# Performance work log

Measured on AMD Instinct MI355X. Metric: run time of the kernel, lower is better.

The kernel has to match this reference:

```python
import jax, jax.numpy as jnp
import numpy as np

B, N, D_DELTA, D_EVT, F, H, L = 4, 2048, 1, 384, 128, 4, 2
NEG_BIG = -9e15

def _gelu(x):
    return jax.nn.gelu(x, approximate=False)

def setup_inputs() -> dict:
    key = jax.random.key(0)
    ks = jax.random.split(key, 32)
    def glorot(k, shape, gain=1.0):
        fan_in, fan_out = shape[-2], shape[-1]
        lim = gain * np.sqrt(6.0 / (fan_in + fan_out))
        return jax.random.uniform(k, shape, jnp.float32, -lim, lim)
    inp = {}
    inp['deltas'] = jax.random.normal(ks[0], (B, N, D_DELTA), jnp.float32)
    inp['event_embeddings'] = jax.random.normal(ks[1], (B, N, D_EVT), jnp.float32)
    u = jax.random.uniform(ks[2], (B, N, N), jnp.float32)
    inp['trade_adjacency'] = jnp.where(u > 0.9, u, 0.0)
    din = D_DELTA + D_EVT
    # message network: din->F, F->F, F->F
    inp['mw1'] = glorot(ks[3], (din, F)); inp['mb1'] = jnp.zeros((F,))
    inp['mw2'] = glorot(ks[4], (F, F));   inp['mb2'] = jnp.zeros((F,))
    inp['mw3'] = glorot(ks[5], (F, F));   inp['mb3'] = jnp.zeros((F,))
    # gate network: din->F//2 -> F
    inp['gw1'] = glorot(ks[6], (din, F // 2)); inp['gb1'] = jnp.zeros((F // 2,))
    inp['gw2'] = glorot(ks[7], (F // 2, F));   inp['gb2'] = jnp.zeros((F,))
    # GAT params per layer/head: W (L,H,F,F), attention vec a split into src/dst halves
    inp['Wg'] = glorot(ks[8], (L, H, F, F), gain=1.414)
    a = glorot(ks[9], (L, H, 2 * F, 1), gain=1.414)
    inp['a_src'] = a[:, :, :F, 0]  # (L,H,F)
    inp['a_dst'] = a[:, :, F:, 0]  # (L,H,F)
    # per-layer head-concat output projection: (L, H*F, F)
    inp['pw'] = glorot(ks[10], (L, H * F, F)); inp['pb'] = jnp.zeros((L, F))
    # output projection: F -> F//2 -> delta_dim
    inp['ow1'] = glorot(ks[11], (F, F // 2)); inp['ob1'] = jnp.zeros((F // 2,))
    inp['ow2'] = glorot(ks[12], (F // 2, D_DELTA)); inp['ob2'] = jnp.zeros((D_DELTA,))
    inp['alpha_param'] = jnp.full((N, D_DELTA), 0.5, jnp.float32)
    inp['beta'] = jnp.asarray(1.0, jnp.float32)
    return inp

def reference(deltas, event_embeddings, trade_adjacency,
              mw1, mb1, mw2, mb2, mw3, mb3, gw1, gb1, gw2, gb2,
              Wg, a_src, a_dst, pw, pb, ow1, ob1, ow2, ob2,
              alpha_param, beta):
    # message function phi(delta, E): gated MLP (eval mode, dropout off)
    combined = jnp.concatenate([deltas, event_embeddings], axis=-1)  # (B,N,din)
    m = _gelu(combined @ mw1 + mb1)
    m = _gelu(m @ mw2 + mb2)
    m = m @ mw3 + mb3
    g = _gelu(combined @ gw1 + gb1)
    g = jax.nn.sigmoid(g @ gw2 + gb2)
    h = m * g  # (B,N,F)
    adj_pos = trade_adjacency[:, None] > 0  # (B,1,N,N)
    for l in range(L):
        Wh = jnp.einsum('bnf,hfo->bhno', h, Wg[l])             # (B,H,N,F)
        s = jnp.einsum('bhno,ho->bhn', Wh, a_src[l])           # score contrib of node i
        t = jnp.einsum('bhno,ho->bhn', Wh, a_dst[l])           # score contrib of node j
        e = jax.nn.leaky_relu(s[:, :, :, None] + t[:, :, None, :], 0.2)  # (B,H,N,N)
        e = jnp.where(adj_pos, e, NEG_BIG)
        attn = jax.nn.softmax(e, axis=-1)
        hp = jax.nn.elu(jnp.einsum('bhij,bhjo->bhio', attn, Wh))  # (B,H,N,F)
        h = hp.transpose(0, 2, 1, 3).reshape(B, N, H * F) @ pw[l] + pb[l]  # (B,N,F)
    prop = _gelu(h @ ow1 + ob1) @ ow2 + ob2                     # (B,N,delta_dim)
    deltas_next = jax.nn.sigmoid(alpha_param)[None] * deltas + beta * prop
    return deltas_next
```

## Files before the change

kernel.cpp:

```cpp
#include <hip/hip_runtime.h>
#include <hip/hip_bf16.h>
#include <math.h>

#define B_ 4
#define N_ 2048
#define F_ 128
#define H_ 4
#define NEG_BIG_F -9.0e15f

typedef float v2 __attribute__((ext_vector_type(2)));
typedef float v4 __attribute__((ext_vector_type(4)));
typedef float f32x16 __attribute__((ext_vector_type(16)));
typedef short s16x8 __attribute__((ext_vector_type(8)));
typedef short s16x4 __attribute__((ext_vector_type(4)));
typedef unsigned u32x4 __attribute__((ext_vector_type(4)));
typedef unsigned u32x2 __attribute__((ext_vector_type(2)));

__device__ __forceinline__ float gelu_f(float x){
  return 0.5f*x*(1.0f+erff(x*0.70710678118654752f));
}
__device__ __forceinline__ float sigmoid_f(float x){
  return 1.0f/(1.0f+__expf(-x));
}
__device__ __forceinline__ short bfbits(float v){
  __hip_bfloat16 h = __float2bfloat16(v);
  short r; __builtin_memcpy(&r, &h, 2); return r;
}
__device__ __forceinline__ float bfback(short s){
  return __uint_as_float(((unsigned)(unsigned short)s) << 16);
}
__device__ __forceinline__ unsigned packhi(float a, float b){
  return __builtin_amdgcn_perm(__float_as_uint(b), __float_as_uint(a), 0x07060302u);
}
__device__ __forceinline__ unsigned cvtpk_bf16(float a, float b){
  unsigned r;
  asm("v_cvt_pk_bf16_f32 %0, %1, %2" : "=v"(r) : "v"(a), "v"(b));
  return r;
}

__global__ void __launch_bounds__(256) mask_kernel(
    const float* __restrict__ adj, unsigned* __restrict__ maskT)
{
  int v = blockIdx.x;
  int b = v >> 6; int n0 = (v & 63) * 32;
  int t = threadIdx.x;
  int r = t >> 3, jg = t & 7;
  __shared__ unsigned mw[32][65];
  const float* arow = adj + (size_t)(b*N_ + n0 + r)*N_;
  for (int wq=0; wq<8; wq++){
    int wdi = jg + 8*wq;
    unsigned bits = 0;
    #pragma unroll
    for (int m=0;m<8;m++){
      v4 a = *(const v4*)(arow + wdi*32 + m*4);
      bits |= (a.x>0.f?1u:0u)<<(m*4);
      bits |= (a.y>0.f?1u:0u)<<(m*4+1);
      bits |= (a.z>0.f?1u:0u)<<(m*4+2);
      bits |= (a.w>0.f?1u:0u)<<(m*4+3);
    }
    mw[r][wdi] = bits;
  }
  __syncthreads();
  #pragma unroll
  for (int q=0;q<8;q++){
    int idx = t + q*256;
    int wdi = idx >> 5, rr = idx & 31;
    maskT[((size_t)b*64 + wdi)*N_ + n0 + rr] = mw[rr][wdi];
  }
}

__global__ void __launch_bounds__(192) w1m_kernel(
    const float* __restrict__ mw1, const float* __restrict__ gw1,
    float* __restrict__ w1m)
{
  int k = blockIdx.x;
  int c = threadIdx.x;
  w1m[(size_t)k*192 + c] = (c < 128) ? mw1[(size_t)k*128 + c]
                                     : gw1[(size_t)k*64 + (c-128)];
}

__global__ void __launch_bounds__(256) mlp1_kernel(
    const float* __restrict__ deltas, const float* __restrict__ evt,
    const float* __restrict__ w1m,
    const float* __restrict__ mb1, const float* __restrict__ gb1,
    float* __restrict__ s1ws)
{
  int row0 = blockIdx.x * 8;
  int t = threadIdx.x;
  int w = t >> 6, l = t & 63;
  int tcol = l & 31, rhalf = l >> 5;
  int c0 = tcol * 6;
  __shared__ float xs[8][392];
  __shared__ float pacc[4][8][192];

  for (int idx = t; idx < 8*385; idx += 256){
    int i = idx / 385;
    int k = idx - i*385;
    xs[i][k] = (k==0) ? deltas[row0+i] : evt[(size_t)(row0+i)*384 + (k-1)];
  }
  __syncthreads();

  int kstart = (w*385) >> 2, kend = ((w+1)*385) >> 2;
  float acc[4][6];
  #pragma unroll
  for (int r=0;r<4;r++)
    #pragma unroll
    for (int e=0;e<6;e++) acc[r][e] = 0.f;

  #pragma unroll 4
  for (int k=kstart; k<kend; k++){
    const float* wp = w1m + (size_t)k*192 + c0;
    v2 wa = *(const v2*)wp;
    v2 wb = *(const v2*)(wp+2);
    v2 wc = *(const v2*)(wp+4);
    #pragma unroll
    for (int r=0;r<4;r++){
      float x = xs[rhalf*4+r][k];
      acc[r][0] += x*wa.x; acc[r][1] += x*wa.y;
      acc[r][2] += x*wb.x; acc[r][3] += x*wb.y;
      acc[r][4] += x*wc.x; acc[r][5] += x*wc.y;
    }
  }
  #pragma unroll
  for (int r=0;r<4;r++){
    float* pp = &pacc[w][rhalf*4+r][c0];
    #pragma unroll
    for (int e=0;e<6;e++) pp[e] = acc[r][e];
  }
  __syncthreads();

  int row = t >> 5, cc0 = (t & 31) * 6;
  #pragma unroll
  for (int e=0;e<6;e++){
    int c = cc0 + e;
    float s = pacc[0][row][c] + pacc[1][row][c] + pacc[2][row][c] + pacc[3][row][c];
    s += (c < 128) ? mb1[c] : gb1[c-128];
    s1ws[(size_t)(row0+row)*192 + c] = gelu_f(s);
  }
}

__global__ void __launch_bounds__(256) mlp2_kernel(
    const float* __restrict__ s1ws,
    const float* __restrict__ mw2, const float* __restrict__ mb2,
    const float* __restrict__ mw3, const float* __restrict__ mb3,
    const float* __restrict__ gw2, const float* __restrict__ gb2,
    float* __restrict__ h_out)
{
  int row0 = blockIdx.x * 8;
  int t = threadIdx.x;
  int w = t >> 6, l = t & 63;
  int tcol = l & 31, rhalf = l >> 5;
  int c0 = tcol * 4;

  __shared__ float sm[1600 + 2048 + 2048 + 1024];
  float (*xs)[200] = (float(*)[200])sm;
  float* mpart = sm + 1600;
  float* gpart = sm + 1600 + 2048;
  float* xs2   = sm + 1600 + 4096;
  float* p3    = sm + 1600;

  for (int idx = t; idx < 8*48; idx += 256){
    int i = idx / 48, c4 = idx - i*48;
    *(v4*)&xs[i][c4*4] = *(const v4*)(s1ws + (size_t)(row0+i)*192 + c4*4);
  }
  __syncthreads();

  {
    v4 acc[4];
    #pragma unroll
    for (int r=0;r<4;r++) acc[r] = (v4)0.f;
    if (w < 2){
      int ks2 = w*64;
      #pragma unroll 4
      for (int k=ks2; k<ks2+64; k++){
        v4 wv = *(const v4*)(mw2 + (size_t)k*128 + c0);
        #pragma unroll
        for (int r=0;r<4;r++) acc[r] += xs[rhalf*4+r][k]*wv;
      }
      #pragma unroll
      for (int r=0;r<4;r++)
        *(v4*)&mpart[((size_t)w*8 + rhalf*4+r)*128 + c0] = acc[r];
    } else {
      int ks2 = (w-2)*32;
      #pragma unroll 4
      for (int k=ks2; k<ks2+32; k++){
        v4 wv = *(const v4*)(gw2 + (size_t)k*128 + c0);
        #pragma unroll
        for (int r=0;r<4;r++) acc[r] += xs[rhalf*4+r][128+k]*wv;
      }
      #pragma unroll
      for (int r=0;r<4;r++)
        *(v4*)&gpart[((size_t)(w-2)*8 + rhalf*4+r)*128 + c0] = acc[r];
    }
  }
  __syncthreads();

  int row = t >> 5, cb = (t & 31) * 4;
  v4 gp;
  {
    v4 m2 = *(const v4*)&mpart[(size_t)row*128 + cb];
    m2 += *(const v4*)&mpart[(size_t)(8+row)*128 + cb];
    m2 += *(const v4*)(mb2 + cb);
    gp = *(const v4*)&gpart[(size_t)row*128 + cb];
    gp += *(const v4*)&gpart[(size_t)(8+row)*128 + cb];
    gp += *(const v4*)(gb2 + cb);
    v4 o;
    o.x = gelu_f(m2.x); o.y = gelu_f(m2.y); o.z = gelu_f(m2.z); o.w = gelu_f(m2.w);
    __syncthreads();
    *(v4*)&xs2[(size_t)row*128 + cb] = o;
  }
  __syncthreads();

  {
    v4 acc3[4];
    #pragma unroll
    for (int r=0;r<4;r++) acc3[r] = (v4)0.f;
    int kc = w*32;
    #pragma unroll 4
    for (int k=kc; k<kc+32; k++){
      v4 wv = *(const v4*)(mw3 + (size_t)k*128 + c0);
      #pragma unroll
      for (int r=0;r<4;r++) acc3[r] += xs2[(size_t)(rhalf*4+r)*128 + k]*wv;
    }
    #pragma unroll
    for (int r=0;r<4;r++)
      *(v4*)&p3[((size_t)w*8 + rhalf*4+r)*128 + c0] = acc3[r];
  }
  __syncthreads();

  {
    v4 s = *(const v4*)&p3[(size_t)row*128 + cb];
    s += *(const v4*)&p3[(size_t)(8+row)*128 + cb];
    s += *(const v4*)&p3[(size_t)(16+row)*128 + cb];
    s += *(const v4*)&p3[(size_t)(24+row)*128 + cb];
    s += *(const v4*)(mb3 + cb);
    v4 o;
    o.x = s.x * sigmoid_f(gp.x);
    o.y = s.y * sigmoid_f(gp.y);
    o.z = s.z * sigmoid_f(gp.z);
    o.w = s.w * sigmoid_f(gp.w);
    *(v4*)(h_out + (size_t)(row0+row)*F_ + cb) = o;
  }
}

__global__ void __launch_bounds__(256) wh_kernel(
    const float* __restrict__ h,
    const float* __restrict__ Wg_l,
    const float* __restrict__ asrc_l,
    const float* __restrict__ adst_l,
    short* __restrict__ WhT_hi,
    float* __restrict__ sArr,
    float* __restrict__ tArr)
{
  int v = blockIdx.x;
  int itile = v & 31;
  int bh = v >> 5;
  int b = bh >> 2, hh = bh & 3;
  int n0 = itile * 64;
  int t = threadIdx.x;
  int i0  = (t & 7) * 8;
  int fo0 = (t >> 3) * 4;

  __shared__ float hT[128][72];
  __shared__ float sP[4][64], tP[4][64];
  for (int idx = t; idx < 64*128; idx += 256){
    int i = idx >> 7, k = idx & 127;
    hT[k][i] = h[(size_t)(b*N_ + n0 + i)*F_ + k];
  }
  __syncthreads();

  const float* W = Wg_l + (size_t)hh*F_*F_;
  v4 accA[4], accB[4];
  #pragma unroll
  for (int c=0;c<4;c++){ accA[c]=(v4)0.f; accB[c]=(v4)0.f; }
  #pragma unroll 4
  for (int k=0;k<F_;k++){
    v4 w = *(const v4*)(W + (size_t)k*F_ + fo0);
    v4 ha = *(const v4*)&hT[k][i0];
    v4 hb = *(const v4*)&hT[k][i0+4];
    accA[0]+=w.x*ha; accA[1]+=w.y*ha; accA[2]+=w.z*ha; accA[3]+=w.w*ha;
    accB[0]+=w.x*hb; accB[1]+=w.y*hb; accB[2]+=w.z*hb; accB[3]+=w.w*hb;
  }
  #pragma unroll
  for (int c=0;c<4;c++){
    s16x8 hi8;
    #pragma unroll
    for (int e=0;e<8;e++){
      float x = (e<4) ? accA[c][e] : accB[c][e-4];
      hi8[e] = bfbits(x);
    }
    size_t off = ((size_t)bh*F_ + fo0 + c)*N_ + n0 + i0;
    *(s16x8*)(WhT_hi + off) = hi8;
  }
  v4 as4 = *(const v4*)(asrc_l + hh*F_ + fo0);
  v4 ad4 = *(const v4*)(adst_l + hh*F_ + fo0);
  v4 sva = accA[0]*as4.x + accA[1]*as4.y + accA[2]*as4.z + accA[3]*as4.w;
  v4 svb = accB[0]*as4.x + accB[1]*as4.y + accB[2]*as4.z + accB[3]*as4.w;
  v4 tva = accA[0]*ad4.x + accA[1]*ad4.y + accA[2]*ad4.z + accA[3]*ad4.w;
  v4 tvb = accB[0]*ad4.x + accB[1]*ad4.y + accB[2]*ad4.z + accB[3]*ad4.w;
  #pragma unroll
  for (int m=8;m<=32;m<<=1){
    sva.x+=__shfl_xor(sva.x,m); sva.y+=__shfl_xor(sva.y,m); sva.z+=__shfl_xor(sva.z,m); sva.w+=__shfl_xor(sva.w,m);
    svb.x+=__shfl_xor(svb.x,m); svb.y+=__shfl_xor(svb.y,m); svb.z+=__shfl_xor(svb.z,m); svb.w+=__shfl_xor(svb.w,m);
    tva.x+=__shfl_xor(tva.x,m); tva.y+=__shfl_xor(tva.y,m); tva.z+=__shfl_xor(tva.z,m); tva.w+=__shfl_xor(tva.w,m);
    tvb.x+=__shfl_xor(tvb.x,m); tvb.y+=__shfl_xor(tvb.y,m); tvb.z+=__shfl_xor(tvb.z,m); tvb.w+=__shfl_xor(tvb.w,m);
  }
  int wv = t >> 6;
  if ((t & 56) == 0){
    *(v4*)&sP[wv][i0] = sva; *(v4*)&sP[wv][i0+4] = svb;
    *(v4*)&tP[wv][i0] = tva; *(v4*)&tP[wv][i0+4] = tvb;
  }
  __syncthreads();
  if (t < 64){
    sArr[(size_t)bh*N_ + n0 + t] = sP[0][t]+sP[1][t]+sP[2][t]+sP[3][t];
    tArr[(size_t)bh*N_ + n0 + t] = tP[0][t]+tP[1][t]+tP[2][t]+tP[3][t];
  }
}

#define WHS 44
#define PBS 18
__global__ void __launch_bounds__(512) attn_kernel(
    const unsigned* __restrict__ maskT,
    const short* __restrict__ WhT_hi,
    const float* __restrict__ sArr,
    const float* __restrict__ tArr,
    float* __restrict__ hpWS)
{
  int v = blockIdx.x;
  int seq = v >> 3, x8 = v & 7;
  int bh = (seq >> 5)*8 + x8;
  int itile = seq & 31;
  int b = bh >> 2;
  int n0 = itile * 64;
  int t = threadIdx.x;
  int w = t >> 6, l = t & 63;
  int lg = l >> 5, ln = l & 31;
  int ihalf = w & 1;
  int ks    = (w >> 1) & 1;
  int fhalf = w >> 2;

  __shared__ float tvecL[N_];
  __shared__ short whHiL[2][128*WHS];
  __shared__ unsigned pbufHi[2][2][32][PBS];
  __shared__ unsigned pbufLo[2][2][32][PBS];
  __shared__ float mxPart[8][64];
  __shared__ float mxL[64], amArgL[64], invL[64];
  __shared__ float lsP[2][4][32];

  const float* tp = tArr + (size_t)bh*N_;
  #pragma unroll
  for (int q=0;q<4;q++) tvecL[t + q*512] = tp[t + q*512];

  s16x8 rh;
  int srow = t >> 2, sseg = t & 3;
  const short* gHi = WhT_hi + (size_t)bh*F_*N_;
  auto STAGE = [&](int jj0){
    size_t o = (size_t)srow*N_ + jj0 + sseg*8;
    rh = *(const s16x8*)(gHi + o);
  };
  auto WRITE = [&](int buf){
    int wo = srow*WHS + sseg*8;
    *(s16x4*)&whHiL[buf][wo]   = __builtin_shufflevector(rh,rh,0,1,2,3);
    *(s16x4*)&whHiL[buf][wo+4] = __builtin_shufflevector(rh,rh,4,5,6,7);
  };

  STAGE(0);
  int il = t & 63, qq = t >> 6;
  float s_il = sArr[(size_t)bh*N_ + n0 + il];
  __syncthreads();

  float mx = NEG_BIG_F;
  const unsigned* mb1p = maskT + (size_t)b*64*N_ + n0;
  for (int wq=0; wq<8; wq++){
    int wdi = qq + wq*8;
    unsigned wd = mb1p[(size_t)wdi*N_ + il];
    while (wd){
      int k2 = __builtin_ctz(wd); wd &= wd - 1;
      float e = s_il + tvecL[wdi*32 + k2];
      e = fmaxf(e, 0.2f*e);
      mx = fmaxf(mx, e);
    }
  }
  mxPart[qq][il] = mx;
  WRITE(0);
  __syncthreads();
  if (t < 64){
    float m = mxPart[0][t];
    #pragma unroll
    for (int q=1;q<8;q++) m = fmaxf(m, mxPart[q][t]);
    bool am = (m <= -8.0e15f);
    mxL[t] = am ? 0.f : m;
    amArgL[t] = am ? 0.f : -1.0e30f;
  }
  __syncthreads();

  int irow = n0 + ihalf*32 + ln;
  float s_lane  = sArr[(size_t)bh*N_ + irow];
  float mx_lane = mxL[ihalf*32 + ln];
  float amArg_lane = amArgL[ihalf*32 + ln];
  const unsigned* mrow = maskT + (size_t)b*64*N_ + irow;

  f32x16 acc0, acc1;
  #pragma unroll
  for (int e2=0;e2<16;e2++){ acc0[e2]=0.f; acc1[e2]=0.f; }
  float lsum = 0.f;

  int jsub = ks*16 + fhalf*8 + lg*4;
  int qidx = jsub >> 1;
  int sh0 = ks*16 + lg*8;

  unsigned mword = mrow[0];
  for (int c=0;c<64;c++){
    int j0 = c*32;
    int cb = c & 1;
    unsigned mword_nx = (c<63) ? mrow[(size_t)(c+1)*N_] : 0u;
    if (c<63) STAGE(j0 + 32);

    {
      v4 tv4 = *(const v4*)&tvecL[j0 + jsub];
      unsigned mm = mword >> jsub;
      float pe0, pe1, pe2, pe3;
      {
        float ev = s_lane + tv4.x; ev = fmaxf(ev, 0.2f*ev);
        pe0 = __expf((mm & 1u) ? (ev - mx_lane) : amArg_lane);
        ev = s_lane + tv4.y; ev = fmaxf(ev, 0.2f*ev);
        pe1 = __expf(((mm>>1) & 1u) ? (ev - mx_lane) : amArg_lane);
        ev = s_lane + tv4.z; ev = fmaxf(ev, 0.2f*ev);
        pe2 = __expf(((mm>>2) & 1u) ? (ev - mx_lane) : amArg_lane);
        ev = s_lane + tv4.w; ev = fmaxf(ev, 0.2f*ev);
        pe3 = __expf(((mm>>3) & 1u) ? (ev - mx_lane) : amArg_lane);
      }
      lsum += (pe0+pe1)+(pe2+pe3);
      u32x2 hiP, loP;
      hiP[0] = packhi(pe0, pe1);
      hiP[1] = packhi(pe2, pe3);
      float l0 = pe0 - __uint_as_float(__float_as_uint(pe0)&0xffff0000u);
      float l1 = pe1 - __uint_as_float(__float_as_uint(pe1)&0xffff0000u);
      float l2 = pe2 - __uint_as_float(__float_as_uint(pe2)&0xffff0000u);
      float l3 = pe3 - __uint_as_float(__float_as_uint(pe3)&0xffff0000u);
      loP[0] = cvtpk_bf16(l0, l1);
      loP[1] = cvtpk_bf16(l2, l3);
      *(u32x2*)&pbufHi[cb][ihalf][ln][qidx] = hiP;
      *(u32x2*)&pbufLo[cb][ihalf][ln][qidx] = loP;
    }
    __syncthreads();

    {
      int aq0 = ks*8 + lg*4;
      u32x2 ha2 = *(const u32x2*)&pbufHi[cb][ihalf][ln][aq0];
      u32x2 hb2 = *(const u32x2*)&pbufHi[cb][ihalf][ln][aq0+2];
      u32x2 la2 = *(const u32x2*)&pbufLo[cb][ihalf][ln][aq0];
      u32x2 lb2 = *(const u32x2*)&pbufLo[cb][ihalf][ln][aq0+2];
      u32x4 h4; h4[0]=ha2[0]; h4[1]=ha2[1]; h4[2]=hb2[0]; h4[3]=hb2[1];
      u32x4 l4; l4[0]=la2[0]; l4[1]=la2[1]; l4[2]=lb2[0]; l4[3]=lb2[1];
      s16x8 ahi = __builtin_bit_cast(s16x8, h4);
      s16x8 alo = __builtin_bit_cast(s16x8, l4);
      __builtin_amdgcn_s_setprio(1);
      #pragma unroll
      for (int aq=0; aq<2; aq++){
        int fr = fhalf*64 + aq*32 + ln;
        const short* bp = &whHiL[cb][fr*WHS + sh0];
        s16x4 b0 = *(const s16x4*)bp;
        s16x4 b1 = *(const s16x4*)(bp+4);
        s16x8 bhi = __builtin_shufflevector(b0,b1,0,1,2,3,4,5,6,7);
        if (aq == 0){
          acc0 = __builtin_amdgcn_mfma_f32_32x32x16_bf16(ahi, bhi, acc0, 0,0,0);
          acc0 = __builtin_amdgcn_mfma_f32_32x32x16_bf16(alo, bhi, acc0, 0,0,0);
        } else {
          acc1 = __builtin_amdgcn_mfma_f32_32x32x16_bf16(ahi, bhi, acc1, 0,0,0);
          acc1 = __builtin_amdgcn_mfma_f32_32x32x16_bf16(alo, bhi, acc1, 0,0,0);
        }
      }
      __builtin_amdgcn_s_setprio(0);
    }
    if (c<63) WRITE(cb ^ 1);
    mword = mword_nx;
  }

  lsum += __shfl_xor(lsum, 32);
  if (l < 32) lsP[ihalf][ks*2+fhalf][l] = lsum;

  float* redbuf = tvecL;
  __syncthreads();
  #pragma unroll
  for (int ihr=0; ihr<2; ihr++){
    if (ks==1 && ihalf==ihr){
      #pragma unroll
      for (int e=0;e<16;e++) redbuf[(fhalf*64 + l)*16 + e] = acc0[e];
    }
    __syncthreads();
    if (ks==0 && ihalf==ihr){
      #pragma unroll
      for (int e=0;e<16;e++) acc0[e] += redbuf[(fhalf*64 + l)*16 + e];
    }
    __syncthreads();
    if (ks==1 && ihalf==ihr){
      #pragma unroll
      for (int e=0;e<16;e++) redbuf[(fhalf*64 + l)*16 + e] = acc1[e];
    }
    __syncthreads();
    if (ks==0 && ihalf==ihr){
      #pragma unroll
      for (int e=0;e<16;e++) acc1[e] += redbuf[(fhalf*64 + l)*16 + e];
    }
    __syncthreads();
  }

  if (t < 64){
    int ih2 = t >> 5, lr = t & 31;
    float s4 = lsP[ih2][0][lr] + lsP[ih2][1][lr] + lsP[ih2][2][lr] + lsP[ih2][3][lr];
    invL[t] = 1.0f / s4;
  }
  __syncthreads();

  if (ks == 0){
    float* hpb = hpWS + ((size_t)bh*N_ + n0 + ihalf*32)*F_ + fhalf*64 + ln;
    #pragma unroll
    for (int q4=0;q4<4;q4++){
      #pragma unroll
      for (int rr=0;rr<4;rr++){
        int r = q4*4+rr;
        int irl = rr + 8*q4 + 4*lg;
        float inv = invL[ihalf*32 + irl];
        float v0 = acc0[r]*inv;
        v0 = v0 > 0.f ? v0 : expm1f(v0);
        hpb[(size_t)irl*F_] = v0;
        float v1 = acc1[r]*inv;
        v1 = v1 > 0.f ? v1 : expm1f(v1);
        hpb[(size_t)irl*F_ + 32] = v1;
      }
    }
  }
}

__global__ void __launch_bounds__(256) proj_kernel(
    const float* __restrict__ hpWS,
    const float* __restrict__ pw_l,
    const float* __restrict__ pb_l,
    float* __restrict__ h_out)
{
  int v = blockIdx.x;
  int b = v >> 8;
  int n0 = (v & 255) * 8;
  int t = threadIdx.x;
  int w = t >> 6, l = t & 63;
  int tcol = l & 31, rhalf = l >> 5;
  int c0 = tcol * 4;

  __shared__ float xsp[4][8][128];
  __shared__ float pacc[4][8][128];
  for (int idx = t; idx < 1024; idx += 256){
    int kh = idx >> 8, r = (idx >> 5) & 7, f4 = idx & 31;
    *(v4*)&xsp[kh][r][f4*4] =
      *(const v4*)(hpWS + ((size_t)(b*H_+kh)*N_ + n0 + r)*F_ + f4*4);
  }
  __syncthreads();

  v4 acc[4];
  #pragma unroll
  for (int r=0;r<4;r++) acc[r] = (v4)0.f;
  const float* pwk = pw_l + (size_t)w*128*F_;
  #pragma unroll 4
  for (int k=0;k<128;k++){
    v4 wv = *(const v4*)(pwk + (size_t)k*F_ + c0);
    #pragma unroll
    for (int r=0;r<4;r++) acc[r] += xsp[w][rhalf*4+r][k]*wv;
  }
  #pragma unroll
  for (int r=0;r<4;r++)
    *(v4*)&pacc[w][rhalf*4+r][c0] = acc[r];
  __syncthreads();

  int row = t >> 5, cb = (t & 31)*4;
  v4 s = *(const v4*)&pacc[0][row][cb];
  s += *(const v4*)&pacc[1][row][cb];
  s += *(const v4*)&pacc[2][row][cb];
  s += *(const v4*)&pacc[3][row][cb];
  s += *(const v4*)(pb_l + cb);
  *(v4*)(h_out + (size_t)(b*N_ + n0 + row)*F_ + cb) = s;
}

__global__ void __launch_bounds__(256) out_kernel(
    const float* __restrict__ h,
    const float* __restrict__ deltas,
    const float* __restrict__ alpha,
    const float* __restrict__ beta,
    const float* __restrict__ ow1, const float* __restrict__ ob1,
    const float* __restrict__ ow2, const float* __restrict__ ob2,
    float* __restrict__ out)
{
  int row0 = blockIdx.x * 32;
  int t = threadIdx.x;
  int il = t >> 3, fg = t & 7;
  int f0 = fg * 8;
  __shared__ float hL[32][132];
  for (int idx = t; idx < 32*128; idx += 256){
    int i = idx >> 7, k = idx & 127;
    hL[i][k] = h[(size_t)(row0+i)*F_ + k];
  }
  __syncthreads();
  float acc[8];
  #pragma unroll
  for (int q=0;q<8;q++) acc[q] = ob1[f0+q];
  for (int k=0;k<F_;k++){
    float c = hL[il][k];
    const float* w = ow1 + (size_t)k*64 + f0;
    v4 wa = *(const v4*)w; v4 wb = *(const v4*)(w+4);
    acc[0]+=c*wa.x; acc[1]+=c*wa.y; acc[2]+=c*wa.z; acc[3]+=c*wa.w;
    acc[4]+=c*wb.x; acc[5]+=c*wb.y; acc[6]+=c*wb.z; acc[7]+=c*wb.w;
  }
  float pp = 0.f;
  #pragma unroll
  for (int q=0;q<8;q++) pp += gelu_f(acc[q]) * ow2[f0+q];
  pp += __shfl_xor(pp, 1);
  pp += __shfl_xor(pp, 2);
  pp += __shfl_xor(pp, 4);
  if (fg == 0){
    int row = row0 + il;
    int n = row & (N_-1);
    float prop = pp + ob2[0];
    out[row] = sigmoid_f(alpha[n]) * deltas[row] + beta[0]*prop;
  }
}

extern "C" void kernel_launch(void* const* d_in, const int* in_sizes, int n_in,
                              void* d_out, int out_size, void* d_ws, size_t ws_size,
                              hipStream_t stream) {
  const float* deltas = (const float*)d_in[0];
  const float* evt    = (const float*)d_in[1];
  const float* adj    = (const float*)d_in[2];
  const float* mw1 = (const float*)d_in[3];
  const float* mb1 = (const float*)d_in[4];
  const float* mw2 = (const float*)d_in[5];
  const float* mb2 = (const float*)d_in[6];
  const float* mw3 = (const float*)d_in[7];
  const float* mb3 = (const float*)d_in[8];
  const float* gw1 = (const float*)d_in[9];
  const float* gb1 = (const float*)d_in[10];
  const float* gw2 = (const float*)d_in[11];
  const float* gb2 = (const float*)d_in[12];
  const float* Wg  = (const float*)d_in[13];
  const float* a_src = (const float*)d_in[14];
  const float* a_dst = (const float*)d_in[15];
  const float* pw = (const float*)d_in[16];
  const float* pb = (const float*)d_in[17];
  const float* ow1 = (const float*)d_in[18];
  const float* ob1 = (const float*)d_in[19];
  const float* ow2 = (const float*)d_in[20];
  const float* ob2 = (const float*)d_in[21];
  const float* alpha = (const float*)d_in[22];
  const float* beta  = (const float*)d_in[23];
  float* out = (float*)d_out;

  float* ws = (float*)d_ws;
  float* hA = ws;
  float* hB = hA + (size_t)B_*N_*F_;
  short* WhT_hi = (short*)(hB + (size_t)B_*N_*F_);
  short* WhT_lo = WhT_hi + (size_t)B_*H_*F_*N_;
  float* hp = (float*)(WhT_lo + (size_t)B_*H_*F_*N_);
  float* sA = hp + (size_t)B_*H_*N_*F_;
  float* tA = sA + (size_t)B_*H_*N_;
  unsigned* maskT = (unsigned*)(tA + (size_t)B_*H_*N_);
  float* w1m = (float*)(maskT + (size_t)B_*64*N_);
  float* s1ws = hp;

  int BN = B_*N_;
  w1m_kernel<<<385, 192, 0, stream>>>(mw1, gw1, w1m);
  mask_kernel<<<B_*64, 256, 0, stream>>>(adj, maskT);
  mlp1_kernel<<<BN/8, 256, 0, stream>>>(deltas, evt, w1m, mb1, gb1, s1ws);
  mlp2_kernel<<<BN/8, 256, 0, stream>>>(s1ws, mw2, mb2, mw3, mb3, gw2, gb2, hA);
  const float* hin = hA; float* hout = hB;
  for (int l=0;l<2;l++){
    wh_kernel<<<16*32, 256, 0, stream>>>(hin,
        Wg + (size_t)l*H_*F_*F_, a_src + (size_t)l*H_*F_, a_dst + (size_t)l*H_*F_,
        WhT_hi, sA, tA);
    attn_kernel<<<512, 512, 0, stream>>>(maskT, WhT_hi, sA, tA, hp);
    proj_kernel<<<1024, 256, 0, stream>>>(hp,
        pw + (size_t)l*H_*F_*F_, pb + (size_t)l*F_, hout);
    float* tmp = (float*)hin; hin = hout; hout = tmp;
  }
  out_kernel<<<BN/32, 256, 0, stream>>>(hin, deltas, alpha, beta, ow1, ob1, ow2, ob2, out);
}
```

Baseline: 295.9 us.

## Fold log2e into attention scores and halve wh_kernel tile for more blocks

In the attention kernel, the t vector is stored twice in shared memory, prescaled by log2e and by 0.2*log2e. Leaky-relu then becomes a max of two affine terms, and the softmax exponent uses raw v_exp_f32 with the row max folded into per-lane constants, which removes multiplies and the expf scaling from the inner loop. Separately, wh_kernel now uses 32-row tiles with 4x4 per-thread outputs and twice as many blocks, aiming for more parallelism on the GPU. The extra t2L array doubles that shared-memory footprint and may reduce occupancy, and each wh block reloads W for fewer rows.

```diff
diff --git a/kernel.cpp b/kernel.cpp
--- a/kernel.cpp
+++ b/kernel.cpp
@@ -7,6 +7,7 @@
 #define F_ 128
 #define H_ 4
 #define NEG_BIG_F -9.0e15f
+#define L2E 1.44269504088896f
 
 typedef float v2 __attribute__((ext_vector_type(2)));
 typedef float v4 __attribute__((ext_vector_type(4)));
@@ -26,15 +27,17 @@
   __hip_bfloat16 h = __float2bfloat16(v);
   short r; __builtin_memcpy(&r, &h, 2); return r;
 }
-__device__ __forceinline__ float bfback(short s){
-  return __uint_as_float(((unsigned)(unsigned short)s) << 16);
-}
 __device__ __forceinline__ unsigned packhi(float a, float b){
   return __builtin_amdgcn_perm(__float_as_uint(b), __float_as_uint(a), 0x07060302u);
 }
 __device__ __forceinline__ unsigned cvtpk_bf16(float a, float b){
   unsigned r;
   asm("v_cvt_pk_bf16_f32 %0, %1, %2" : "=v"(r) : "v"(a), "v"(b));
+  return r;
+}
+__device__ __forceinline__ float exp2_f(float x){
+  float r;
+  asm("v_exp_f32 %0, %1" : "=v"(r) : "v"(x));
   return r;
 }
 
@@ -253,65 +256,63 @@
     float* __restrict__ tArr)
 {
   int v = blockIdx.x;
-  int itile = v & 31;
-  int bh = v >> 5;
+  int itile = v & 63;
+  int bh = v >> 6;
   int b = bh >> 2, hh = bh & 3;
-  int n0 = itile * 64;
+  int n0 = itile * 32;
   int t = threadIdx.x;
-  int i0  = (t & 7) * 8;
-  int fo0 = (t >> 3) * 4;
-
-  __shared__ float hT[128][72];
-  __shared__ float sP[4][64], tP[4][64];
-  for (int idx = t; idx < 64*128; idx += 256){
+  int w = t >> 6;
+  int ig = t & 7;
+  int fg = t >> 3;
+  int i0 = ig*4, f0 = fg*4;
+
+  __shared__ float hT[128][36];
+  __shared__ float sP[4][32], tP[4][32];
+  for (int idx = t; idx < 32*128; idx += 256){
     int i = idx >> 7, k = idx & 127;
     hT[k][i] = h[(size_t)(b*N_ + n0 + i)*F_ + k];
   }
   __syncthreads();
 
   const float* W = Wg_l + (size_t)hh*F_*F_;
-  v4 accA[4], accB[4];
-  #pragma unroll
-  for (int c=0;c<4;c++){ accA[c]=(v4)0.f; accB[c]=(v4)0.f; }
+  v4 acc[4];
+  #pragma unroll
+  for (int r=0;r<4;r++) acc[r] = (v4)0.f;
   #pragma unroll 4
   for (int k=0;k<F_;k++){
-    v4 w = *(const v4*)(W + (size_t)k*F_ + fo0);
-    v4 ha = *(const v4*)&hT[k][i0];
-    v4 hb = *(const v4*)&hT[k][i0+4];
-    accA[0]+=w.x*ha; accA[1]+=w.y*ha; accA[2]+=w.z*ha; accA[3]+=w.w*ha;
-    accB[0]+=w.x*hb; accB[1]+=w.y*hb; accB[2]+=w.z*hb; accB[3]+=w.w*hb;
+    v4 wv = *(const v4*)(W + (size_t)k*F_ + f0);
+    v4 hv = *(const v4*)&hT[k][i0];
+    acc[0] += hv.x*wv; acc[1] += hv.y*wv; acc[2] += hv.z*wv; acc[3] += hv.w*wv;
   }
   #pragma unroll
   for (int c=0;c<4;c++){
-    s16x8 hi8;
-    #pragma unroll
-    for (int e=0;e<8;e++){
-      float x = (e<4) ? accA[c][e] : accB[c][e-4];
-      hi8[e] = bfbits(x);
-    }
-    size_t off = ((size_t)bh*F_ + fo0 + c)*N_ + n0 + i0;
-    *(s16x8*)(WhT_hi + off) = hi8;
-  }
-  v4 as4 = *(const v4*)(asrc_l + hh*F_ + fo0);
-  v4 ad4 = *(const v4*)(adst_l + hh*F_ + fo0);
-  v4 sva = accA[0]*as4.x + accA[1]*as4.y + accA[2]*as4.z + accA[3]*as4.w;
-  v4 svb = accB[0]*as4.x + accB[1]*as4.y + accB[2]*as4.z + accB[3]*as4.w;
-  v4 tva = accA[0]*ad4.x + accA[1]*ad4.y + accA[2]*ad4.z + accA[3]*ad4.w;
-  v4 tvb = accB[0]*ad4.x + accB[1]*ad4.y + accB[2]*ad4.z + accB[3]*ad4.w;
+    s16x4 hi4;
+    #pragma unroll
+    for (int e=0;e<4;e++) hi4[e] = bfbits(acc[e][c]);
+    *(s16x4*)(WhT_hi + ((size_t)bh*F_ + f0 + c)*N_ + n0 + i0) = hi4;
+  }
+  v4 as4 = *(const v4*)(asrc_l + hh*F_ + f0);
+  v4 ad4 = *(const v4*)(adst_l + hh*F_ + f0);
+  float sv[4], tv[4];
+  #pragma unroll
+  for (int r=0;r<4;r++){
+    sv[r] = acc[r].x*as4.x + acc[r].y*as4.y + acc[r].z*as4.z + acc[r].w*as4.w;
+    tv[r] = acc[r].x*ad4.x + acc[r].y*ad4.y + acc[r].z*ad4.z + acc[r].w*ad4.w;
+  }
   #pragma unroll
   for (int m=8;m<=32;m<<=1){
-    sva.x+=__shfl_xor(sva.x,m); sva.y+=__shfl_xor(sva.y,m); sva.z+=__shfl_xor(sva.z,m); sva.w+=__shfl_xor(sva.w,m);
-    svb.x+=__shfl_xor(svb.x,m); svb.y+=__shfl_xor(svb.y,m); svb.z+=__shfl_xor(svb.z,m); svb.w+=__shfl_xor(svb.w,m);
-    tva.x+=__shfl_xor(tva.x,m); tva.y+=__shfl_xor(tva.y,m); tva.z+=__shfl_xor(tva.z,m); tva.w+=__shfl_xor(tva.w,m);
-    tvb.x+=__shfl_xor(tvb.x,m); tvb.y+=__shfl_xor(tvb.y,m); tvb.z+=__shfl_xor(tvb.z,m); tvb.w+=__shfl_xor(tvb.w,m);
-  }
-  int wv = t >> 6;
+    #pragma unroll
+    for (int r=0;r<4;r++){
+      sv[r] += __shfl_xor(sv[r], m);
+      tv[r] += __shfl_xor(tv[r], m);
+    }
+  }
   if ((t & 56) == 0){
-    *(v4*)&sP[wv][i0] = sva; *(v4*)&sP[wv][i0+4] = svb;
-    *(v4*)&tP[wv][i0] = tva; *(v4*)&tP[wv][i0+4] = tvb;
-  }
-  __syncthreads();
-  if (t < 64){
+    #pragma unroll
+    for (int r=0;r<4;r++){ sP[w][i0+r] = sv[r]; tP[w][i0+r] = tv[r]; }
+  }
+  __syncthreads();
+  if (t < 32){
     sArr[(size_t)bh*N_ + n0 + t] = sP[0][t]+sP[1][t]+sP[2][t]+sP[3][t];
     tArr[(size_t)bh*N_ + n0 + t] = tP[0][t]+tP[1][t]+tP[2][t]+tP[3][t];
   }
@@ -339,7 +340,8 @@
   int ks    = (w >> 1) & 1;
   int fhalf = w >> 2;
 
-  __shared__ float tvecL[N_];
+  __shared__ float t1L[N_];
+  __shared__ float t2L[N_];
   __shared__ short whHiL[2][128*WHS];
   __shared__ unsigned pbufHi[2][2][32][PBS];
   __shared__ unsigned pbufLo[2][2][32][PBS];
@@ -349,7 +351,11 @@
 
   const float* tp = tArr + (size_t)bh*N_;
   #pragma unroll
-  for (int q=0;q<4;q++) tvecL[t + q*512] = tp[t + q*512];
+  for (int q=0;q<4;q++){
+    float tvv = tp[t + q*512];
+    t1L[t + q*512] = tvv * L2E;
+    t2L[t + q*512] = tvv * (0.2f*L2E);
+  }
 
   s16x8 rh;
   int srow = t >> 2, sseg = t & 3;
@@ -367,6 +373,7 @@
   STAGE(0);
   int il = t & 63, qq = t >> 6;
   float s_il = sArr[(size_t)bh*N_ + n0 + il];
+  float s1_il = s_il * L2E, s2_il = s_il * (0.2f*L2E);
   __syncthreads();
 
   float mx = NEG_BIG_F;
@@ -376,8 +383,7 @@
     unsigned wd = mb1p[(size_t)wdi*N_ + il];
     while (wd){
       int k2 = __builtin_ctz(wd); wd &= wd - 1;
-      float e = s_il + tvecL[wdi*32 + k2];
-      e = fmaxf(e, 0.2f*e);
+      float e = fmaxf(s1_il + t1L[wdi*32 + k2], s2_il + t2L[wdi*32 + k2]);
       mx = fmaxf(mx, e);
     }
   }
@@ -398,6 +404,8 @@
   float s_lane  = sArr[(size_t)bh*N_ + irow];
   float mx_lane = mxL[ihalf*32 + ln];
   float amArg_lane = amArgL[ihalf*32 + ln];
+  float Ac = s_lane*L2E - mx_lane;
+  float Bc = s_lane*(0.2f*L2E) - mx_lane;
   const unsigned* mrow = maskT + (size_t)b*64*N_ + irow;
 
   f32x16 acc0, acc1;
@@ -417,19 +425,17 @@
     if (c<63) STAGE(j0 + 32);
 
     {
-      v4 tv4 = *(const v4*)&tvecL[j0 + jsub];
+      v4 ta1 = *(const v4*)&t1L[j0 + jsub];
+      v4 ta2 = *(const v4*)&t2L[j0 + jsub];
       unsigned mm = mword >> jsub;
-      float pe0, pe1, pe2, pe3;
-      {
-        float ev = s_lane + tv4.x; ev = fmaxf(ev, 0.2f*ev);
-        pe0 = __expf((mm & 1u) ? (ev - mx_lane) : amArg_lane);
-        ev = s_lane + tv4.y; ev = fmaxf(ev, 0.2f*ev);
-        pe1 = __expf(((mm>>1) & 1u) ? (ev - mx_lane) : amArg_lane);
-        ev = s_lane + tv4.z; ev = fmaxf(ev, 0.2f*ev);
-        pe2 = __expf(((mm>>2) & 1u) ? (ev - mx_lane) : amArg_lane);
-        ev = s_lane + tv4.w; ev = fmaxf(ev, 0.2f*ev);
-        pe3 = __expf(((mm>>3) & 1u) ? (ev - mx_lane) : amArg_lane);
-      }
+      float a0 = fmaxf(Ac + ta1.x, Bc + ta2.x);
+      float a1 = fmaxf(Ac + ta1.y, Bc + ta2.y);
+      float a2 = fmaxf(Ac + ta1.z, Bc + ta2.z);
+      float a3 = fmaxf(Ac + ta1.w, Bc + ta2.w);
+      float pe0 = exp2_f((mm & 1u)      ? a0 : amArg_lane);
+      float pe1 = exp2_f(((mm>>1) & 1u) ? a1 : amArg_lane);
+      float pe2 = exp2_f(((mm>>2) & 1u) ? a2 : amArg_lane);
+      float pe3 = exp2_f(((mm>>3) & 1u) ? a3 : amArg_lane);
       lsum += (pe0+pe1)+(pe2+pe3);
       u32x2 hiP, loP;
       hiP[0] = packhi(pe0, pe1);
@@ -480,7 +486,7 @@
   lsum += __shfl_xor(lsum, 32);
   if (l < 32) lsP[ihalf][ks*2+fhalf][l] = lsum;
 
-  float* redbuf = tvecL;
+  float* redbuf = t1L;
   __syncthreads();
   #pragma unroll
   for (int ihr=0; ihr<2; ihr++){
@@ -671,7 +677,7 @@
   mlp2_kernel<<<BN/8, 256, 0, stream>>>(s1ws, mw2, mb2, mw3, mb3, gw2, gb2, hA);
   const float* hin = hA; float* hout = hB;
   for (int l=0;l<2;l++){
-    wh_kernel<<<16*32, 256, 0, stream>>>(hin,
+    wh_kernel<<<16*64, 256, 0, stream>>>(hin,
         Wg + (size_t)l*H_*F_*F_, a_src + (size_t)l*H_*F_, a_dst + (size_t)l*H_*F_,
         WhT_hi, sA, tA);
     attn_kernel<<<512, 512, 0, stream>>>(maskT, WhT_hi, sA, tA, hp);
```

Result: slower. 304.4 us (+2.9%).

## Fuse last projection with output MLP and fold leaky-relu exp into exp2

Applied to the files above, without the earlier changes.

The attention kernel now precomputes the t vector scaled by log2(e) and by 0.2*log2(e), so each score becomes a max of two fused adds followed by a raw v_exp_f32. This replaces the add, max, subtract and __expf sequence in the inner softmax loop. The final layer's head projection is fused with the output MLP into one kernel, which drops a launch and the round trip of h through global memory. In exchange the kernel uses an extra 8KB of shared memory per block, the output MLP runs at lower parallelism per row, and the rounding of the softmax terms changes slightly.

```diff
diff --git a/kernel.cpp b/kernel.cpp
--- a/kernel.cpp
+++ b/kernel.cpp
@@ -7,6 +7,7 @@
 #define F_ 128
 #define H_ 4
 #define NEG_BIG_F -9.0e15f
+#define L2E 1.44269504088896f
 
 typedef float v2 __attribute__((ext_vector_type(2)));
 typedef float v4 __attribute__((ext_vector_type(4)));
@@ -26,15 +27,17 @@
   __hip_bfloat16 h = __float2bfloat16(v);
   short r; __builtin_memcpy(&r, &h, 2); return r;
 }
-__device__ __forceinline__ float bfback(short s){
-  return __uint_as_float(((unsigned)(unsigned short)s) << 16);
-}
 __device__ __forceinline__ unsigned packhi(float a, float b){
   return __builtin_amdgcn_perm(__float_as_uint(b), __float_as_uint(a), 0x07060302u);
 }
 __device__ __forceinline__ unsigned cvtpk_bf16(float a, float b){
   unsigned r;
   asm("v_cvt_pk_bf16_f32 %0, %1, %2" : "=v"(r) : "v"(a), "v"(b));
+  return r;
+}
+__device__ __forceinline__ float exp2_f(float x){
+  float r;
+  asm("v_exp_f32 %0, %1" : "=v"(r) : "v"(x));
   return r;
 }
 
@@ -339,7 +342,8 @@
   int ks    = (w >> 1) & 1;
   int fhalf = w >> 2;
 
-  __shared__ float tvecL[N_];
+  __shared__ float t1L[N_];
+  __shared__ float t2L[N_];
   __shared__ short whHiL[2][128*WHS];
   __shared__ unsigned pbufHi[2][2][32][PBS];
   __shared__ unsigned pbufLo[2][2][32][PBS];
@@ -349,7 +353,11 @@
 
   const float* tp = tArr + (size_t)bh*N_;
   #pragma unroll
-  for (int q=0;q<4;q++) tvecL[t + q*512] = tp[t + q*512];
+  for (int q=0;q<4;q++){
+    float tvv = tp[t + q*512];
+    t1L[t + q*512] = tvv * L2E;
+    t2L[t + q*512] = tvv * (0.2f*L2E);
+  }
 
   s16x8 rh;
   int srow = t >> 2, sseg = t & 3;
@@ -367,6 +375,7 @@
   STAGE(0);
   int il = t & 63, qq = t >> 6;
   float s_il = sArr[(size_t)bh*N_ + n0 + il];
+  float s1_il = s_il * L2E, s2_il = s_il * (0.2f*L2E);
   __syncthreads();
 
   float mx = NEG_BIG_F;
@@ -376,8 +385,7 @@
     unsigned wd = mb1p[(size_t)wdi*N_ + il];
     while (wd){
       int k2 = __builtin_ctz(wd); wd &= wd - 1;
-      float e = s_il + tvecL[wdi*32 + k2];
-      e = fmaxf(e, 0.2f*e);
+      float e = fmaxf(s1_il + t1L[wdi*32 + k2], s2_il + t2L[wdi*32 + k2]);
       mx = fmaxf(mx, e);
     }
   }
@@ -398,6 +406,8 @@
   float s_lane  = sArr[(size_t)bh*N_ + irow];
   float mx_lane = mxL[ihalf*32 + ln];
   float amArg_lane = amArgL[ihalf*32 + ln];
+  float Ac = s_lane*L2E - mx_lane;
+  float Bc = s_lane*(0.2f*L2E) - mx_lane;
   const unsigned* mrow = maskT + (size_t)b*64*N_ + irow;
 
   f32x16 acc0, acc1;
@@ -417,19 +427,17 @@
     if (c<63) STAGE(j0 + 32);
 
     {
-      v4 tv4 = *(const v4*)&tvecL[j0 + jsub];
+      v4 ta1 = *(const v4*)&t1L[j0 + jsub];
+      v4 ta2 = *(const v4*)&t2L[j0 + jsub];
       unsigned mm = mword >> jsub;
-      float pe0, pe1, pe2, pe3;
-      {
-        float ev = s_lane + tv4.x; ev = fmaxf(ev, 0.2f*ev);
-        pe0 = __expf((mm & 1u) ? (ev - mx_lane) : amArg_lane);
-        ev = s_lane + tv4.y; ev = fmaxf(ev, 0.2f*ev);
-        pe1 = __expf(((mm>>1) & 1u) ? (ev - mx_lane) : amArg_lane);
-        ev = s_lane + tv4.z; ev = fmaxf(ev, 0.2f*ev);
-        pe2 = __expf(((mm>>2) & 1u) ? (ev - mx_lane) : amArg_lane);
-        ev = s_lane + tv4.w; ev = fmaxf(ev, 0.2f*ev);
-        pe3 = __expf(((mm>>3) & 1u) ? (ev - mx_lane) : amArg_lane);
-      }
+      float a0 = fmaxf(Ac + ta1.x, Bc + ta2.x);
+      float a1 = fmaxf(Ac + ta1.y, Bc + ta2.y);
+      float a2 = fmaxf(Ac + ta1.z, Bc + ta2.z);
+      float a3 = fmaxf(Ac + ta1.w, Bc + ta2.w);
+      float pe0 = exp2_f((mm & 1u)      ? a0 : amArg_lane);
+      float pe1 = exp2_f(((mm>>1) & 1u) ? a1 : amArg_lane);
+      float pe2 = exp2_f(((mm>>2) & 1u) ? a2 : amArg_lane);
+      float pe3 = exp2_f(((mm>>3) & 1u) ? a3 : amArg_lane);
       lsum += (pe0+pe1)+(pe2+pe3);
       u32x2 hiP, loP;
       hiP[0] = packhi(pe0, pe1);
@@ -480,7 +488,7 @@
   lsum += __shfl_xor(lsum, 32);
   if (l < 32) lsP[ihalf][ks*2+fhalf][l] = lsum;
 
-  float* redbuf = tvecL;
+  float* redbuf = t1L;
   __syncthreads();
   #pragma unroll
   for (int ihr=0; ihr<2; ihr++){
@@ -580,8 +588,10 @@
   *(v4*)(h_out + (size_t)(b*N_ + n0 + row)*F_ + cb) = s;
 }
 
-__global__ void __launch_bounds__(256) out_kernel(
-    const float* __restrict__ h,
+__global__ void __launch_bounds__(256) proj_out_kernel(
+    const float* __restrict__ hpWS,
+    const float* __restrict__ pw_l,
+    const float* __restrict__ pb_l,
     const float* __restrict__ deltas,
     const float* __restrict__ alpha,
     const float* __restrict__ beta,
@@ -589,37 +599,70 @@
     const float* __restrict__ ow2, const float* __restrict__ ob2,
     float* __restrict__ out)
 {
-  int row0 = blockIdx.x * 32;
+  int v = blockIdx.x;
+  int b = v >> 8;
+  int n0 = (v & 255) * 8;
   int t = threadIdx.x;
-  int il = t >> 3, fg = t & 7;
-  int f0 = fg * 8;
-  __shared__ float hL[32][132];
-  for (int idx = t; idx < 32*128; idx += 256){
-    int i = idx >> 7, k = idx & 127;
-    hL[i][k] = h[(size_t)(row0+i)*F_ + k];
-  }
-  __syncthreads();
-  float acc[8];
-  #pragma unroll
-  for (int q=0;q<8;q++) acc[q] = ob1[f0+q];
+  int w = t >> 6, l = t & 63;
+  int tcol = l & 31, rhalf = l >> 5;
+  int c0 = tcol * 4;
+
+  __shared__ float xsp[4][8][128];
+  __shared__ float pacc[4][8][128];
+  for (int idx = t; idx < 1024; idx += 256){
+    int kh = idx >> 8, r = (idx >> 5) & 7, f4 = idx & 31;
+    *(v4*)&xsp[kh][r][f4*4] =
+      *(const v4*)(hpWS + ((size_t)(b*H_+kh)*N_ + n0 + r)*F_ + f4*4);
+  }
+  __syncthreads();
+
+  v4 acc[4];
+  #pragma unroll
+  for (int r=0;r<4;r++) acc[r] = (v4)0.f;
+  const float* pwk = pw_l + (size_t)w*128*F_;
+  #pragma unroll 4
+  for (int k=0;k<128;k++){
+    v4 wv = *(const v4*)(pwk + (size_t)k*F_ + c0);
+    #pragma unroll
+    for (int r=0;r<4;r++) acc[r] += xsp[w][rhalf*4+r][k]*wv;
+  }
+  #pragma unroll
+  for (int r=0;r<4;r++)
+    *(v4*)&pacc[w][rhalf*4+r][c0] = acc[r];
+  __syncthreads();
+
+  int row = t >> 5, cb = (t & 31)*4;
+  {
+    v4 s = *(const v4*)&pacc[0][row][cb];
+    s += *(const v4*)&pacc[1][row][cb];
+    s += *(const v4*)&pacc[2][row][cb];
+    s += *(const v4*)&pacc[3][row][cb];
+    s += *(const v4*)(pb_l + cb);
+    *(v4*)&xsp[0][row][cb] = s;
+  }
+  __syncthreads();
+
+  int il = t >> 5;
+  int c2 = (t & 31) * 2;
+  float u0 = ob1[c2], u1 = ob1[c2+1];
+  const float* hr = xsp[0][il];
+  #pragma unroll 4
   for (int k=0;k<F_;k++){
-    float c = hL[il][k];
-    const float* w = ow1 + (size_t)k*64 + f0;
-    v4 wa = *(const v4*)w; v4 wb = *(const v4*)(w+4);
-    acc[0]+=c*wa.x; acc[1]+=c*wa.y; acc[2]+=c*wa.z; acc[3]+=c*wa.w;
-    acc[4]+=c*wb.x; acc[5]+=c*wb.y; acc[6]+=c*wb.z; acc[7]+=c*wb.w;
-  }
-  float pp = 0.f;
-  #pragma unroll
-  for (int q=0;q<8;q++) pp += gelu_f(acc[q]) * ow2[f0+q];
+    float hv = hr[k];
+    v2 wv = *(const v2*)(ow1 + (size_t)k*64 + c2);
+    u0 += hv*wv.x; u1 += hv*wv.y;
+  }
+  float pp = gelu_f(u0)*ow2[c2] + gelu_f(u1)*ow2[c2+1];
   pp += __shfl_xor(pp, 1);
   pp += __shfl_xor(pp, 2);
   pp += __shfl_xor(pp, 4);
-  if (fg == 0){
-    int row = row0 + il;
-    int n = row & (N_-1);
+  pp += __shfl_xor(pp, 8);
+  pp += __shfl_xor(pp, 16);
+  if ((t & 31) == 0){
+    int n = n0 + il;
+    size_t rowg = (size_t)b*N_ + n;
     float prop = pp + ob2[0];
-    out[row] = sigmoid_f(alpha[n]) * deltas[row] + beta[0]*prop;
+    out[rowg] = sigmoid_f(alpha[n]) * deltas[rowg] + beta[0]*prop;
   }
 }
 
@@ -669,15 +712,17 @@
   mask_kernel<<<B_*64, 256, 0, stream>>>(adj, maskT);
   mlp1_kernel<<<BN/8, 256, 0, stream>>>(deltas, evt, w1m, mb1, gb1, s1ws);
   mlp2_kernel<<<BN/8, 256, 0, stream>>>(s1ws, mw2, mb2, mw3, mb3, gw2, gb2, hA);
-  const float* hin = hA; float* hout = hB;
-  for (int l=0;l<2;l++){
-    wh_kernel<<<16*32, 256, 0, stream>>>(hin,
-        Wg + (size_t)l*H_*F_*F_, a_src + (size_t)l*H_*F_, a_dst + (size_t)l*H_*F_,
-        WhT_hi, sA, tA);
-    attn_kernel<<<512, 512, 0, stream>>>(maskT, WhT_hi, sA, tA, hp);
-    proj_kernel<<<1024, 256, 0, stream>>>(hp,
-        pw + (size_t)l*H_*F_*F_, pb + (size_t)l*F_, hout);
-    float* tmp = (float*)hin; hin = hout; hout = tmp;
-  }
-  out_kernel<<<BN/32, 256, 0, stream>>>(hin, deltas, alpha, beta, ow1, ob1, ow2, ob2, out);
-}
+
+  wh_kernel<<<16*32, 256, 0, stream>>>(hA,
+      Wg, a_src, a_dst, WhT_hi, sA, tA);
+  attn_kernel<<<512, 512, 0, stream>>>(maskT, WhT_hi, sA, tA, hp);
+  proj_kernel<<<1024, 256, 0, stream>>>(hp, pw, pb, hB);
+
+  wh_kernel<<<16*32, 256, 0, stream>>>(hB,
+      Wg + (size_t)H_*F_*F_, a_src + (size_t)H_*F_, a_dst + (size_t)H_*F_,
+      WhT_hi, sA, tA);
+  attn_kernel<<<512, 512, 0, stream>>>(maskT, WhT_hi, sA, tA, hp);
+  proj_out_kernel<<<1024, 256, 0, stream>>>(hp,
+      pw + (size_t)H_*F_*F_, pb + (size_t)F_,
+      deltas, alpha, beta, ow1, ob1, ow2, ob2, out);
+}
```

Result: no change. 293.3 us (-0.9%).
